# Kernel optimization log

Measured on AMD Instinct MI355X. Metric: run time of the kernel, lower is better.

Reference implementation:

```python
import jax, jax.numpy as jnp
import numpy as np

N, D = 10000, 20
NODE_DIM = 172
D_T = 172
EDGE_DIM = 172
N_HEAD = 2
D_MODEL = NODE_DIM + EDGE_DIM + D_T  # 516


def _layer_norm(x, g, b, eps=1e-5):
    mu = jnp.mean(x, axis=-1, keepdims=True)
    var = jnp.mean((x - mu) ** 2, axis=-1, keepdims=True)
    return (x - mu) / jnp.sqrt(var + eps) * g + b


def setup_inputs() -> dict:
    key = jax.random.key(0)
    ks = jax.random.split(key, 12)
    d_k = D_MODEL // N_HEAD
    std_qk = np.sqrt(2.0 / (D_MODEL + d_k)).astype(np.float32)
    node_h = jax.random.normal(ks[0], (N, NODE_DIM), jnp.float32)
    edge_t = jax.random.uniform(ks[1], (N, D), jnp.float32, 0.0, 100.0)
    edge_feat = jax.random.normal(ks[2], (N, D, EDGE_DIM), jnp.float32)
    nbr_idx = jax.random.randint(ks[3], (N, D), 0, N)
    t_now = jnp.array([100.0], jnp.float32)
    # weights stored [in, out]; apply as x @ W
    w_q = jax.random.normal(ks[4], (D_MODEL, N_HEAD * d_k), jnp.float32) * std_qk
    w_k = jax.random.normal(ks[5], (D_MODEL, N_HEAD * d_k), jnp.float32) * std_qk
    w_v = jax.random.normal(ks[6], (D_MODEL, N_HEAD * d_k), jnp.float32) * std_qk
    basis_freq = jnp.asarray(1.0 / 10 ** np.linspace(0, 9, D_T), jnp.float32)
    phase = jnp.zeros((D_T,), jnp.float32)
    ln_gamma = jnp.ones((D_MODEL,), jnp.float32)
    ln_beta = jnp.zeros((D_MODEL,), jnp.float32)
    fc_w = jax.random.normal(ks[7], (N_HEAD * d_k, D_MODEL), jnp.float32) * np.float32(np.sqrt(2.0 / (N_HEAD * d_k + D_MODEL)))
    fc_b = jnp.zeros((D_MODEL,), jnp.float32)
    m1_w = jax.random.normal(ks[8], (D_MODEL + NODE_DIM, NODE_DIM), jnp.float32) * np.float32(np.sqrt(2.0 / (D_MODEL + 2 * NODE_DIM)))
    m1_b = jnp.zeros((NODE_DIM,), jnp.float32)
    m2_w = jax.random.normal(ks[9], (NODE_DIM, NODE_DIM), jnp.float32) * np.float32(np.sqrt(1.0 / NODE_DIM))
    m2_b = jnp.zeros((NODE_DIM,), jnp.float32)
    return dict(node_h=node_h, edge_t=edge_t, edge_feat=edge_feat, nbr_idx=nbr_idx,
                t_now=t_now, n_head=N_HEAD, w_q=w_q, w_k=w_k, w_v=w_v,
                basis_freq=basis_freq, phase=phase, ln_gamma=ln_gamma, ln_beta=ln_beta,
                fc_w=fc_w, fc_b=fc_b, m1_w=m1_w, m1_b=m1_b, m2_w=m2_w, m2_b=m2_b)


def reference(node_h, edge_t, edge_feat, nbr_idx, t_now, n_head, w_q, w_k, w_v,
              basis_freq, phase, ln_gamma, ln_beta, fc_w, fc_b, m1_w, m1_b, m2_w, m2_b):
    n, deg = edge_t.shape
    d_model = w_q.shape[0]
    d_t = basis_freq.shape[0]
    edge_dim = d_model - node_h.shape[1] - d_t
    d_k = d_model // n_head
    # message_func: per-edge cosine time encoding + k/v projections
    t_enc = jnp.cos((t_now[0] - edge_t)[..., None] * basis_freq + phase)  # [N,D,d_T]
    z = jnp.concatenate([node_h[nbr_idx], edge_feat, t_enc], axis=-1)     # [N,D,d_model]
    k = z @ w_k                                                            # [N,D,H*dk]
    v = z @ w_v
    # reduce_func: self query (zero edge feat, cos(phase) time enc)
    self_z = jnp.concatenate([node_h,
                              jnp.zeros((n, edge_dim), node_h.dtype),
                              jnp.ones((n, d_t), node_h.dtype) * jnp.cos(phase)], axis=-1)
    q = self_z @ w_q                                                       # [N,H*dk]
    # reproduce the exact torch permute/view sequence (head-major flatten)
    qh = q.reshape(n, 1, n_head, d_k).transpose(2, 0, 1, 3).reshape(-1, 1, d_model)
    kh = k.reshape(n, deg, n_head, d_k).transpose(2, 0, 1, 3).reshape(-1, deg, d_model)
    vh = v.reshape(n, deg, n_head, d_k).transpose(2, 0, 1, 3).reshape(-1, deg, d_model)
    attn = jnp.einsum('bqd,bkd->bqk', qh, kh) / jnp.asarray(d_k ** 0.5, qh.dtype)
    attn = jax.nn.softmax(attn, axis=2)
    out = jnp.einsum('bqk,bkd->bqd', attn, vh)                             # [N,1,d_model]
    out = out[:, 0, :].reshape(n_head, n, d_k).transpose(1, 0, 2).reshape(n, -1)
    out = out @ fc_w + fc_b                                                # attn_fc (dropout in eval)
    h = _layer_norm(out + self_z, ln_gamma, ln_beta)
    # merger MLP
    x = jnp.concatenate([h, node_h], axis=-1)
    return jax.nn.relu(x @ m1_w + m1_b) @ m2_w + m2_b
```

## Files before the change

kernel.cpp:

```cpp
#include <hip/hip_runtime.h>
#include <hip/hip_bf16.h>
#include <math.h>

typedef __bf16 bf16;
typedef __attribute__((ext_vector_type(4))) __bf16 bf16x4;
typedef __attribute__((ext_vector_type(8))) __bf16 bf16x8;
typedef __attribute__((ext_vector_type(4))) float f32x4;

constexpr int NN   = 10000;
constexpr int NPAD = 10112;
constexpr int BN = 176, BK = 64;

constexpr size_t FCWT_OFF = 0;
constexpr size_t M1WT_OFF = 608256;
constexpr size_t M2WT_OFF = 856064;
constexpr size_t WKH_OFF  = 923648;
constexpr size_t WQHT_OFF = 1660928;
constexpr size_t WVH_OFF  = 2111488;
constexpr size_t WQKT_OFF = 3012608;
constexpr size_t WVFT_OFF = 3485696;
constexpr size_t QB_OFF   = 4702208;
constexpr size_t QKB_OFF  = 4706304;
constexpr size_t CPH_OFF  = 4714496;
constexpr size_t NH16_OFF = 4715520;
constexpr size_t QK_OFF   = NH16_OFF + (size_t)NPAD*192*2;
constexpr size_t ZB_OFF   = QK_OFF   + (size_t)NPAD*1152*2;
constexpr size_t FCR_OFF  = ZB_OFF   + (size_t)NPAD*1152*2;
constexpr size_t X_OFF    = FCR_OFF  + (size_t)NN*516*4;
constexpr size_t R_OFF    = X_OFF    + (size_t)NPAD*704*2;

typedef __attribute__((address_space(3))) void lds_void;
typedef const __attribute__((address_space(1))) void glb_void;
__device__ __forceinline__ void gload16(const void* g, void* l) {
    __builtin_amdgcn_global_load_lds((glb_void*)(uintptr_t)g,
                                     (lds_void*)(unsigned int)(uintptr_t)l, 16, 0, 0);
}

__global__ __launch_bounds__(256)
void packT_kernel(const float* __restrict__ fcw, const float* __restrict__ m1w,
                  const float* __restrict__ m2w,
                  bf16* __restrict__ FCWT, bf16* __restrict__ M1WT, bf16* __restrict__ M2WT) {
    __shared__ float tile[32][33];
    const float* src; bf16* dst; int K, C, LD;
    switch (blockIdx.y) {
        case 0:  src = fcw; K = 516; C = 516; dst = FCWT; LD = 576; break;
        case 1:  src = m1w; K = 688; C = 172; dst = M1WT; LD = 704; break;
        default: src = m2w; K = 172; C = 172; dst = M2WT; LD = 192; break;
    }
    const int tilesC = (C + 31) >> 5, tilesK = (K + 31) >> 5;
    const int nt = tilesC * tilesK;
    const int tx = threadIdx.x & 31, ty = threadIdx.x >> 5;
    for (int tb = blockIdx.x; tb < nt; tb += gridDim.x) {
        int tc = tb % tilesC, tk = tb / tilesC;
        #pragma unroll
        for (int i = 0; i < 4; ++i) {
            int k = tk*32 + ty + i*8, c = tc*32 + tx;
            tile[ty + i*8][tx] = (k < K && c < C) ? src[(size_t)k*C + c] : 0.f;
        }
        __syncthreads();
        #pragma unroll
        for (int i = 0; i < 4; ++i) {
            int c = tc*32 + ty + i*8, k = tk*32 + tx;
            if (c < C && k < K) dst[(size_t)c*LD + k] = (bf16)tile[tx][ty + i*8];
        }
        __syncthreads();
    }
}

__global__ void pack_misc_kernel(const float* __restrict__ wk, const float* __restrict__ wq,
                                 const float* __restrict__ wv, const float* __restrict__ node_h,
                                 const float* __restrict__ phase,
                                 bf16* __restrict__ WKH, bf16* __restrict__ WQHT,
                                 bf16* __restrict__ WVH, bf16* __restrict__ nh16,
                                 float* __restrict__ cph) {
    constexpr int T0 = 2*516*258;
    constexpr int T1 = T0 + 2*172*258;
    constexpr int T2 = T1 + 2*516*258;
    constexpr int T3 = T2 + NN*192;
    constexpr int T4 = T3 + 172;
    for (int idx = blockIdx.x * blockDim.x + threadIdx.x; idx < T4;
         idx += gridDim.x * blockDim.x) {
        if (idx < T0) {
            int h = idx / (516*258), rem = idx % (516*258), d = rem / 258, j = rem % 258;
            WKH[((size_t)h*576 + d)*320 + j] = (bf16)wk[(size_t)d*516 + h*258 + j];
        } else if (idx < T1) {
            int i = idx - T0;
            int h = i / (172*258), rem = i % (172*258), k = rem / 258, j = rem % 258;
            WQHT[((size_t)h*352 + k)*320 + j] = (bf16)wq[(size_t)k*516 + h*258 + j];
        } else if (idx < T2) {
            int i = idx - T1;
            int h = i / (516*258), rem = i % (516*258), c = rem / 258, j = rem % 258;
            WVH[((size_t)h*704 + c)*320 + j] = (bf16)wv[(size_t)c*516 + h*258 + j];
        } else if (idx < T3) {
            int i = idx - T2, r = i / 192, c = i % 192;
            nh16[i] = (c < 172) ? (bf16)node_h[(size_t)r*172 + c] : (bf16)0.f;
        } else cph[idx - T3] = cosf(phase[idx - T3]);
    }
}

__global__ __launch_bounds__(256)
void qbias_kernel(const float* __restrict__ w_q, const float* __restrict__ phase,
                  float* __restrict__ q_bias) {
    __shared__ float red[256];
    const int c = blockIdx.x, j = threadIdx.x;
    red[j] = (j < 172) ? cosf(phase[j]) * w_q[(size_t)(344 + j) * 516 + c] : 0.f;
    __syncthreads();
    #pragma unroll
    for (int o = 128; o; o >>= 1) { if (j < o) red[j] += red[j + o]; __syncthreads(); }
    if (j == 0) q_bias[c] = red[0];
}

__global__ __launch_bounds__(256)
void qkb_kernel(const float* __restrict__ wk, const float* __restrict__ QB,
                float* __restrict__ qkb) {
    __shared__ float red[256];
    const int hd = blockIdx.x, h = hd / 576, d = hd % 576, t = threadIdx.x;
    float a = 0.f;
    if (d < 516) {
        a = QB[h*258 + t] * wk[(size_t)d*516 + h*258 + t];
        if (t < 2) a += QB[h*258 + 256 + t] * wk[(size_t)d*516 + h*258 + 256 + t];
    }
    red[t] = a; __syncthreads();
    #pragma unroll
    for (int o = 128; o; o >>= 1) { if (t < o) red[t] += red[t + o]; __syncthreads(); }
    if (t == 0) qkb[hd] = red[0];
}

template<int KP, int EPI, int MT>
__global__ __launch_bounds__(256, 2)
void gemm_kernel(const bf16* __restrict__ A, int lda, const bf16* __restrict__ Bt,
                 float* __restrict__ outF, bf16* __restrict__ outB, int ldo,
                 const float* __restrict__ bias,
                 const float* __restrict__ aux0, const float* __restrict__ aux1,
                 int Mreal, int Nreal) {
    constexpr int NT  = KP / BK;
    constexpr int BMt = 64 * MT;
    __shared__ __align__(16) bf16 As[2][BMt][BK];
    __shared__ __align__(16) bf16 Bs[2][BN][BK];

    const int tid  = threadIdx.x;
    const int w    = tid >> 6;
    const int lane = tid & 63;
    const int lr   = lane & 15;
    const int ls   = lane >> 4;
    const int lrow = lane >> 3;
    const int lcol = (lane & 7) * 8;

    const bf16* aBase = A  + (size_t)(blockIdx.y * BMt + w * 16 * MT + lrow) * lda + lcol;
    const bf16* bBase = Bt + (size_t)(blockIdx.x * BN + lrow) * KP + lcol;

    auto stage = [&](int buf, int k0) {
        #pragma unroll
        for (int i = 0; i < 2 * MT; ++i)
            gload16(aBase + (size_t)(i * 8) * lda + k0, &As[buf][w * 16 * MT + i * 8][0]);
        #pragma unroll
        for (int jj = 0; jj < 6; ++jj) {
            int j = jj * 4 + w;
            if (j < 22) gload16(bBase + (size_t)(j * 8) * KP + k0, &Bs[buf][j * 8][0]);
        }
    };

    f32x4 acc[MT][11];
    #pragma unroll
    for (int a = 0; a < MT; ++a)
        #pragma unroll
        for (int b2 = 0; b2 < 11; ++b2) acc[a][b2] = (f32x4)(0.0f);

    stage(0, 0);
    __syncthreads();
    int cur = 0;
    for (int t = 0; t < NT; ++t) {
        if (t + 1 < NT) stage(cur ^ 1, (t + 1) * BK);
        #pragma unroll
        for (int kk = 0; kk < 2; ++kk) {
            bf16x8 afr[MT];
            #pragma unroll
            for (int mt = 0; mt < MT; ++mt)
                afr[mt] = *(const bf16x8*)&As[cur][w*16*MT + mt*16 + lr][kk*32 + ls*8];
            #pragma unroll
            for (int nt = 0; nt < 11; ++nt) {
                bf16x8 bfr = *(const bf16x8*)&Bs[cur][nt*16 + lr][kk*32 + ls*8];
                #pragma unroll
                for (int mt = 0; mt < MT; ++mt)
                    acc[mt][nt] = __builtin_amdgcn_mfma_f32_16x16x32_bf16(afr[mt], bfr, acc[mt][nt], 0, 0, 0);
            }
        }
        __syncthreads();
        cur ^= 1;
    }

    const int colb = blockIdx.x * BN + lr;
    const int rowb = blockIdx.y * BMt + w*16*MT + ls*4;
    #pragma unroll
    for (int mt = 0; mt < MT; ++mt)
    #pragma unroll
    for (int nt = 0; nt < 11; ++nt)
    #pragma unroll
    for (int q2 = 0; q2 < 4; ++q2) {
        int row = rowb + mt*16 + q2;
        int col = colb + nt*16;
        if (row >= Mreal) continue;
        float v = acc[mt][nt][q2];
        if constexpr (EPI == 0) {
            if (col < Nreal) outB[(size_t)row*ldo + col] = (bf16)(v + bias[col]);
        } else if constexpr (EPI == 2) {
            if (col < Nreal) {
                float sz = (col < 172) ? aux0[(size_t)row*172 + col]
                                       : ((col < 344) ? 0.f : aux1[col - 344]);
                outF[(size_t)row*ldo + col] = v + bias[col] + sz;
            }
        } else if constexpr (EPI == 3) {
            float vv = (col < Nreal) ? fmaxf(v + bias[col], 0.f) : 0.f;
            outB[(size_t)row*ldo + col] = (bf16)vv;
        } else {
            if (col < Nreal) outF[(size_t)row*ldo + col] = v + bias[col];
        }
    }
}

__global__ __launch_bounds__(256, 2)
void gemm_multi_kernel(const bf16* __restrict__ WKH, const bf16* __restrict__ WQHT,
                       const bf16* __restrict__ FCWT, const bf16* __restrict__ WVH,
                       bf16* __restrict__ WQKT, bf16* __restrict__ WVFT) {
    constexpr int KP = 320, NT = KP / BK;
    const int z = blockIdx.z, h = z & 1;
    const bf16 *A, *Bt; bf16* outB; int lda, ldo, Mreal, Nreal;
    if (z < 2) {
        if (blockIdx.x >= 2) return;
        A = WKH + (size_t)h*576*320;  lda = 320;
        Bt = WQHT + (size_t)h*352*320;
        outB = WQKT + (size_t)h*576*192; ldo = 192; Mreal = 576; Nreal = 192;
    } else {
        A = FCWT + (size_t)h*258;     lda = 576;
        Bt = WVH + (size_t)h*704*320;
        outB = WVFT + (size_t)h*576;  ldo = 1152; Mreal = 516; Nreal = 576;
    }
    __shared__ __align__(16) bf16 As[2][128][BK];
    __shared__ __align__(16) bf16 Bs[2][BN][BK];
    const int tid = threadIdx.x, w = tid >> 6, lane = tid & 63;
    const int lr = lane & 15, ls = lane >> 4;
    const int lrow = lane >> 3, lcol = (lane & 7) * 8;
    const bf16* aBase = A  + (size_t)(blockIdx.y * 128 + w * 32 + lrow) * lda + lcol;
    const bf16* bBase = Bt + (size_t)(blockIdx.x * BN + lrow) * KP + lcol;
    auto stage = [&](int buf, int k0) {
        #pragma unroll
        for (int i = 0; i < 4; ++i)
            gload16(aBase + (size_t)(i * 8) * lda + k0, &As[buf][w * 32 + i * 8][0]);
        #pragma unroll
        for (int jj = 0; jj < 6; ++jj) {
            int j = jj * 4 + w;
            if (j < 22) gload16(bBase + (size_t)(j * 8) * KP + k0, &Bs[buf][j * 8][0]);
        }
    };
    f32x4 acc[2][11];
    #pragma unroll
    for (int a = 0; a < 2; ++a)
        #pragma unroll
        for (int b2 = 0; b2 < 11; ++b2) acc[a][b2] = (f32x4)(0.0f);
    stage(0, 0);
    __syncthreads();
    int cur = 0;
    for (int t = 0; t < NT; ++t) {
        if (t + 1 < NT) stage(cur ^ 1, (t + 1) * BK);
        #pragma unroll
        for (int kk = 0; kk < 2; ++kk) {
            bf16x8 a0 = *(const bf16x8*)&As[cur][w*32 +      lr][kk*32 + ls*8];
            bf16x8 a1 = *(const bf16x8*)&As[cur][w*32 + 16 + lr][kk*32 + ls*8];
            #pragma unroll
            for (int nt = 0; nt < 11; ++nt) {
                bf16x8 bfr = *(const bf16x8*)&Bs[cur][nt*16 + lr][kk*32 + ls*8];
                acc[0][nt] = __builtin_amdgcn_mfma_f32_16x16x32_bf16(a0, bfr, acc[0][nt], 0, 0, 0);
                acc[1][nt] = __builtin_amdgcn_mfma_f32_16x16x32_bf16(a1, bfr, acc[1][nt], 0, 0, 0);
            }
        }
        __syncthreads();
        cur ^= 1;
    }
    const int colb = blockIdx.x * BN + lr;
    const int rowb = blockIdx.y * 128 + w*32 + ls*4;
    #pragma unroll
    for (int mt = 0; mt < 2; ++mt)
    #pragma unroll
    for (int nt = 0; nt < 11; ++nt)
    #pragma unroll
    for (int q2 = 0; q2 < 4; ++q2) {
        int row = rowb + mt*16 + q2;
        int col = colb + nt*16;
        if (row < Mreal && col < Nreal)
            outB[(size_t)row*ldo + col] = (bf16)acc[mt][nt][q2];
    }
}

__global__ __launch_bounds__(256, 3)
void attn_lite_kernel(const bf16* __restrict__ QK, const bf16* __restrict__ nh16,
                      const float* __restrict__ edge_feat, const float* __restrict__ edge_t,
                      const int* __restrict__ nbr_idx, const float* __restrict__ freq,
                      const float* __restrict__ ph, const float* __restrict__ tnow,
                      bf16* __restrict__ ZB) {
    __shared__ __align__(16) bf16 zs[40 * 576];
    __shared__ __align__(16) float G[40][4];
    __shared__ float sfreq[172], sph[172];
    __shared__ float sdt[40];
    __shared__ int   ssrc[40];
    __shared__ float pp[2][20];

    const int r  = blockIdx.x;
    const int iA = 2 * r;
    const int t  = threadIdx.x;
    const int w  = t >> 6, lane = t & 63;
    const int lr = lane & 15, ls = lane >> 4;

    auto zsa = [&](int row, int c) -> bf16* {
        unsigned b = (unsigned)(row * 1152 + c * 2) ^ (unsigned)((row & 7) << 4);
        return (bf16*)((char*)zs + b);
    };

    f32x4 efA[4], efB[4];
    #pragma unroll
    for (int s = 0; s < 4; ++s) {
        int idx = t + (s + 3) * 256;
        if (idx >= 880 && idx < 1720) {
            int i2 = idx - 880;
            int row = i2 / 21, c = 22 + i2 % 21;
            const float* ep = edge_feat + (size_t)(iA * 20 + row) * 172 + (c * 8 - 172);
            efA[s] = *(const f32x4*)ep;
            efB[s] = *(const f32x4*)(ep + 4);
        }
    }

    if (t < 172) { sfreq[t] = freq[t]; sph[t] = ph[t]; }
    if (t >= 192 && t < 232) {
        int e2 = t - 192, ge = iA * 20 + e2;
        sdt[e2]  = tnow[0] - edge_t[ge];
        ssrc[e2] = nbr_idx[ge];
    }
    __syncthreads();

    #pragma unroll
    for (int it = 0; it < 4; ++it) {
        int idx = t + it * 256;
        if (idx < 880) {
            int row = idx / 22, c = idx % 22;
            bf16x8 v;
            if (c < 21) {
                v = *(const bf16x8*)(nh16 + (size_t)ssrc[row] * 192 + c * 8);
            } else {
                int ge = iA * 20 + row;
                #pragma unroll
                for (int e = 0; e < 8; ++e) {
                    int k = 168 + e;
                    v[e] = (k < 172) ? nh16[(size_t)ssrc[row] * 192 + k]
                                     : (bf16)edge_feat[(size_t)ge * 172 + (k - 172)];
                }
            }
            *(bf16x8*)zsa(row, c * 8) = v;
        }
    }
    #pragma unroll
    for (int it = 6; it < 12; ++it) {
        int idx = t + it * 256;
        if (idx >= 1720 && idx < 2880) {
            int row, c;
            bf16x8 v;
            if (idx < 2600) {
                int i3 = idx - 1720;
                row = i3 / 22; c = 43 + i3 % 22;
                float dt = sdt[row];
                int k0 = c * 8;
                #pragma unroll
                for (int e = 0; e < 8; ++e) {
                    int k = k0 + e;
                    v[e] = (k < 516) ? (bf16)__cosf(dt * sfreq[k - 344] + sph[k - 344]) : (bf16)0.f;
                }
            } else {
                int i4 = idx - 2600;
                row = i4 / 7; c = 65 + i4 % 7;
                #pragma unroll
                for (int e = 0; e < 8; ++e) v[e] = (bf16)0.f;
            }
            *(bf16x8*)zsa(row, c * 8) = v;
        }
    }
    #pragma unroll
    for (int s = 0; s < 4; ++s) {
        int idx = t + (s + 3) * 256;
        if (idx >= 880 && idx < 1720) {
            int i2 = idx - 880;
            int row = i2 / 21, c = 22 + i2 % 21;
            bf16x8 v;
            #pragma unroll
            for (int e = 0; e < 4; ++e) { v[e] = (bf16)efA[s][e]; v[e+4] = (bf16)efB[s][e]; }
            *(bf16x8*)zsa(row, c * 8) = v;
        }
    }
    __syncthreads();

    if (w < 3) {
        int brow = w * 16 + lr; if (brow > 39) brow = 39;
        const bf16* aQK = QK + (size_t)(iA + ((lr >> 1) & 1)) * 1152 + (lane & 1) * 576;
        f32x4 acc = (f32x4)(0.0f);
        __builtin_amdgcn_s_setprio(1);
        #pragma unroll
        for (int ks = 0; ks < 18; ++ks) {
            bf16x8 af = *(const bf16x8*)(aQK + ks * 32 + ls * 8);
            bf16x8 bf = *(const bf16x8*)zsa(brow, ks * 32 + ls * 8);
            acc = __builtin_amdgcn_mfma_f32_16x16x32_bf16(af, bf, acc, 0, 0, 0);
        }
        __builtin_amdgcn_s_setprio(0);
        int col = w * 16 + lr;
        if (ls == 0 && col < 40) *(f32x4*)&G[col][0] = acc;
    }
    __syncthreads();

    if (t < 64) {
        int h = lane >> 5, knbr = lane & 31;
        bool act = knbr < 20;
        float l = -1e30f;
        if (act) {
            int z0 = (knbr / 10) * 20 + 2 * (knbr % 10);
            l = (G[z0][h] + G[z0 + 1][2 + h]) * 0.0622573006f;
        }
        float m = l;
        #pragma unroll
        for (int o = 16; o >= 1; o >>= 1) m = fmaxf(m, __shfl_xor(m, o));
        float e = act ? __expf(l - m) : 0.f;
        float s2 = e;
        #pragma unroll
        for (int o = 16; o >= 1; o >>= 1) s2 += __shfl_xor(s2, o);
        if (act) pp[h][knbr] = e / s2;
    }
    __syncthreads();

    #pragma unroll
    for (int it = 0; it < 2; ++it) {
        int idx = t + it * 256;
        if (idx < 288) {
            int nsel = idx / 144, c4 = (idx % 144) * 4;
            float a0[4] = {0.f, 0.f, 0.f, 0.f};
            float a1[4] = {0.f, 0.f, 0.f, 0.f};
            #pragma unroll
            for (int knbr = 0; knbr < 20; ++knbr) {
                int z0 = (knbr / 10) * 20 + 2 * (knbr % 10) + nsel;
                bf16x4 zv = *(const bf16x4*)zsa(z0, c4);
                float p0 = pp[0][knbr], p1 = pp[1][knbr];
                #pragma unroll
                for (int i = 0; i < 4; ++i) {
                    float zf = (float)zv[i];
                    a0[i] += p0 * zf;
                    a1[i] += p1 * zf;
                }
            }
            bf16x4 o0, o1;
            #pragma unroll
            for (int i = 0; i < 4; ++i) { o0[i] = (bf16)a0[i]; o1[i] = (bf16)a1[i]; }
            *(bf16x4*)(ZB + (size_t)(iA + nsel) * 1152 + c4)       = o0;
            *(bf16x4*)(ZB + (size_t)(iA + nsel) * 1152 + 576 + c4) = o1;
        }
    }
}

__global__ __launch_bounds__(256)
void ln_x_kernel(const float* __restrict__ fcr, const float* __restrict__ g,
                 const float* __restrict__ b, const bf16* __restrict__ nh16,
                 bf16* __restrict__ X) {
    __shared__ float red[2][4];
    __shared__ float mb[2];
    const size_t i = blockIdx.x;
    const int t = threadIdx.x;
    int c0 = t, c1 = t + 256, c2 = t + 512;
    float v0 = fcr[i*516 + c0];
    float v1 = (c1 < 516) ? fcr[i*516 + c1] : 0.f;
    float v2 = (c2 < 516) ? fcr[i*516 + c2] : 0.f;
    float s = v0 + v1 + v2, ss = v0*v0 + v1*v1 + v2*v2;
    #pragma unroll
    for (int o = 32; o; o >>= 1) { s += __shfl_down(s, o); ss += __shfl_down(ss, o); }
    if ((t & 63) == 0) { red[0][t >> 6] = s; red[1][t >> 6] = ss; }
    __syncthreads();
    if (t == 0) {
        float S  = red[0][0] + red[0][1] + red[0][2] + red[0][3];
        float SS = red[1][0] + red[1][1] + red[1][2] + red[1][3];
        float mean = S / 516.f;
        float var  = SS / 516.f - mean*mean;
        mb[0] = mean; mb[1] = rsqrtf(var + 1e-5f);
    }
    __syncthreads();
    float mean = mb[0], rstd = mb[1];
    X[i*704 + c0] = (bf16)((v0 - mean)*rstd*g[c0] + b[c0]);
    if (c1 < 516) X[i*704 + c1] = (bf16)((v1 - mean)*rstd*g[c1] + b[c1]);
    if (c2 < 516) X[i*704 + c2] = (bf16)((v2 - mean)*rstd*g[c2] + b[c2]);
    for (int c = 516 + t; c < 704; c += 256)
        X[i*704 + c] = (c < 688) ? nh16[i*192 + (c - 516)] : (bf16)0.f;
}

extern "C" void kernel_launch(void* const* d_in, const int* in_sizes, int n_in,
                              void* d_out, int out_size, void* d_ws, size_t ws_size,
                              hipStream_t stream) {
    const float* node_h     = (const float*)d_in[0];
    const float* edge_t     = (const float*)d_in[1];
    const float* edge_feat  = (const float*)d_in[2];
    const int*   nbr_idx    = (const int*)d_in[3];
    const float* t_now      = (const float*)d_in[4];
    const float* w_q        = (const float*)d_in[6];
    const float* w_k        = (const float*)d_in[7];
    const float* w_v        = (const float*)d_in[8];
    const float* basis_freq = (const float*)d_in[9];
    const float* phase      = (const float*)d_in[10];
    const float* ln_g       = (const float*)d_in[11];
    const float* ln_b       = (const float*)d_in[12];
    const float* fc_w       = (const float*)d_in[13];
    const float* fc_b       = (const float*)d_in[14];
    const float* m1_w       = (const float*)d_in[15];
    const float* m1_b       = (const float*)d_in[16];
    const float* m2_w       = (const float*)d_in[17];
    const float* m2_b       = (const float*)d_in[18];

    char* ws = (char*)d_ws;
    bf16*  FCWT = (bf16*)(ws + FCWT_OFF);
    bf16*  M1WT = (bf16*)(ws + M1WT_OFF);
    bf16*  M2WT = (bf16*)(ws + M2WT_OFF);
    bf16*  WKH  = (bf16*)(ws + WKH_OFF);
    bf16*  WQHT = (bf16*)(ws + WQHT_OFF);
    bf16*  WVH  = (bf16*)(ws + WVH_OFF);
    bf16*  WQKT = (bf16*)(ws + WQKT_OFF);
    bf16*  WVFT = (bf16*)(ws + WVFT_OFF);
    float* QB   = (float*)(ws + QB_OFF);
    float* QKB  = (float*)(ws + QKB_OFF);
    float* CPH  = (float*)(ws + CPH_OFF);
    bf16*  NH16 = (bf16*)(ws + NH16_OFF);
    bf16*  QK   = (bf16*)(ws + QK_OFF);
    bf16*  ZB   = (bf16*)(ws + ZB_OFF);
    float* FCR  = (float*)(ws + FCR_OFF);
    bf16*  Xb   = (bf16*)(ws + X_OFF);
    bf16*  Rb   = (bf16*)(ws + R_OFF);

    hipMemsetAsync(ws, 0, NH16_OFF, stream);

    packT_kernel<<<dim3(289, 3), 256, 0, stream>>>(fc_w, m1_w, m2_w, FCWT, M1WT, M2WT);
    pack_misc_kernel<<<2048, 256, 0, stream>>>(w_k, w_q, w_v, node_h, phase,
                                               WKH, WQHT, WVH, NH16, CPH);
    qbias_kernel<<<516, 256, 0, stream>>>(w_q, phase, QB);
    qkb_kernel<<<1152, 256, 0, stream>>>(w_k, QB, QKB);

    gemm_multi_kernel<<<dim3(4, 5, 4), 256, 0, stream>>>(WKH, WQHT, FCWT, WVH, WQKT, WVFT);

    gemm_kernel<192, 0, 1><<<dim3(7, 158), 256, 0, stream>>>(
        NH16, 192, WQKT, nullptr, QK, 1152, QKB, nullptr, nullptr, NN, 1152);

    attn_lite_kernel<<<NN / 2, 256, 0, stream>>>(
        QK, NH16, edge_feat, edge_t, nbr_idx, basis_freq, phase, t_now, ZB);

    gemm_kernel<1152, 2, 1><<<dim3(3, 158), 256, 0, stream>>>(
        ZB, 1152, WVFT, FCR, nullptr, 516, fc_b, node_h, CPH, NN, 516);

    ln_x_kernel<<<NN, 256, 0, stream>>>(FCR, ln_g, ln_b, NH16, Xb);

    gemm_kernel<704, 3, 1><<<dim3(1, 158), 256, 0, stream>>>(
        Xb, 704, M1WT, nullptr, Rb, 192, m1_b, nullptr, nullptr, NN, 172);

    gemm_kernel<192, 4, 1><<<dim3(1, 158), 256, 0, stream>>>(
        Rb, 192, M2WT, (float*)d_out, nullptr, 172, m2_b, nullptr, nullptr, NN, 172);
}
```

Measured before the change: 251.0 us.

## Stage QK rows in shared memory and fold qbias into pack kernel

The attention kernel now loads the four QK half-rows for its two nodes into a swizzled shared-memory buffer once, and the MFMA loop reads the A operand from there instead of repeatedly fetching it from global memory per lane. Separately, the standalone qbias reduction kernel is removed and its work is done as a serial 172-term loop per output inside the grid-stride pack_misc kernel, saving one launch. The serial loop puts long-latency strided loads on a few threads, which may extend the tail of pack_misc, and the extra shared buffer could reduce occupancy slightly.

Measured after the change: 286.9 us. 14.3% more time.

```diff
diff --git a/kernel.cpp b/kernel.cpp
--- a/kernel.cpp
+++ b/kernel.cpp
@@ -72,13 +72,14 @@
                                  const float* __restrict__ phase,
                                  bf16* __restrict__ WKH, bf16* __restrict__ WQHT,
                                  bf16* __restrict__ WVH, bf16* __restrict__ nh16,
-                                 float* __restrict__ cph) {
+                                 float* __restrict__ cph, float* __restrict__ QB) {
     constexpr int T0 = 2*516*258;
     constexpr int T1 = T0 + 2*172*258;
     constexpr int T2 = T1 + 2*516*258;
     constexpr int T3 = T2 + NN*192;
     constexpr int T4 = T3 + 172;
-    for (int idx = blockIdx.x * blockDim.x + threadIdx.x; idx < T4;
+    constexpr int T5 = T4 + 516;
+    for (int idx = blockIdx.x * blockDim.x + threadIdx.x; idx < T5;
          idx += gridDim.x * blockDim.x) {
         if (idx < T0) {
             int h = idx / (516*258), rem = idx % (516*258), d = rem / 258, j = rem % 258;
@@ -94,20 +95,16 @@
         } else if (idx < T3) {
             int i = idx - T2, r = i / 192, c = i % 192;
             nh16[i] = (c < 172) ? (bf16)node_h[(size_t)r*172 + c] : (bf16)0.f;
-        } else cph[idx - T3] = cosf(phase[idx - T3]);
-    }
-}
-
-__global__ __launch_bounds__(256)
-void qbias_kernel(const float* __restrict__ w_q, const float* __restrict__ phase,
-                  float* __restrict__ q_bias) {
-    __shared__ float red[256];
-    const int c = blockIdx.x, j = threadIdx.x;
-    red[j] = (j < 172) ? cosf(phase[j]) * w_q[(size_t)(344 + j) * 516 + c] : 0.f;
-    __syncthreads();
-    #pragma unroll
-    for (int o = 128; o; o >>= 1) { if (j < o) red[j] += red[j + o]; __syncthreads(); }
-    if (j == 0) q_bias[c] = red[0];
+        } else if (idx < T4) {
+            cph[idx - T3] = cosf(phase[idx - T3]);
+        } else {
+            int c = idx - T4;
+            float s = 0.f;
+            for (int j = 0; j < 172; ++j)
+                s += cosf(phase[j]) * wq[(size_t)(344 + j) * 516 + c];
+            QB[c] = s;
+        }
+    }
 }
 
 __global__ __launch_bounds__(256)
@@ -298,6 +295,7 @@
                       const float* __restrict__ ph, const float* __restrict__ tnow,
                       bf16* __restrict__ ZB) {
     __shared__ __align__(16) bf16 zs[40 * 576];
+    __shared__ __align__(16) bf16 qks[4 * 576];
     __shared__ __align__(16) float G[40][4];
     __shared__ float sfreq[172], sph[172];
     __shared__ float sdt[40];
@@ -314,6 +312,20 @@
         unsigned b = (unsigned)(row * 1152 + c * 2) ^ (unsigned)((row & 7) << 4);
         return (bf16*)((char*)zs + b);
     };
+    auto qka = [&](int row, int c) -> bf16* {
+        unsigned b = (unsigned)(row * 1152 + c * 2) ^ (unsigned)((row & 3) << 5);
+        return (bf16*)((char*)qks + b);
+    };
+
+    #pragma unroll
+    for (int s = 0; s < 2; ++s) {
+        int idx = t + s * 256;
+        if (idx < 288) {
+            int m = idx / 72, g = idx % 72;
+            *(bf16x8*)qka(m, g * 8) =
+                *(const bf16x8*)(QK + (size_t)(iA + (m >> 1)) * 1152 + (m & 1) * 576 + g * 8);
+        }
+    }
 
     f32x4 efA[4], efB[4];
     #pragma unroll
@@ -397,12 +409,11 @@
 
     if (w < 3) {
         int brow = w * 16 + lr; if (brow > 39) brow = 39;
-        const bf16* aQK = QK + (size_t)(iA + ((lr >> 1) & 1)) * 1152 + (lane & 1) * 576;
         f32x4 acc = (f32x4)(0.0f);
         __builtin_amdgcn_s_setprio(1);
         #pragma unroll
         for (int ks = 0; ks < 18; ++ks) {
-            bf16x8 af = *(const bf16x8*)(aQK + ks * 32 + ls * 8);
+            bf16x8 af = *(const bf16x8*)qka(lr & 3, ks * 32 + ls * 8);
             bf16x8 bf = *(const bf16x8*)zsa(brow, ks * 32 + ls * 8);
             acc = __builtin_amdgcn_mfma_f32_16x16x32_bf16(af, bf, acc, 0, 0, 0);
         }
@@ -537,8 +548,7 @@
 
     packT_kernel<<<dim3(289, 3), 256, 0, stream>>>(fc_w, m1_w, m2_w, FCWT, M1WT, M2WT);
     pack_misc_kernel<<<2048, 256, 0, stream>>>(w_k, w_q, w_v, node_h, phase,
-                                               WKH, WQHT, WVH, NH16, CPH);
-    qbias_kernel<<<516, 256, 0, stream>>>(w_q, phase, QB);
+                                               WKH, WQHT, WVH, NH16, CPH, QB);
     qkb_kernel<<<1152, 256, 0, stream>>>(w_k, QB, QKB);
 
     gemm_multi_kernel<<<dim3(4, 5, 4), 256, 0, stream>>>(WKH, WQHT, FCWT, WVH, WQKT, WVFT);
```
